# Kernel tuning notes

Measured on AMD Instinct MI355X. Metric: run time of the kernel, lower is better.

The kernel has to match this reference:

```python
import jax, jax.numpy as jnp
import numpy as np

N = 50000      # nodes
E = 800000     # edges
C_IN = 128
C_HID = 128
C_OUT = 128
LN_EPS = 1e-5  # PyG LayerNorm default eps


def setup_inputs() -> dict:
    key = jax.random.key(0)
    ks = jax.random.split(key, 8)
    x = jax.random.normal(ks[0], (N, C_IN), jnp.float32)
    edge_index = jax.random.randint(ks[1], (2, E), 0, N, dtype=jnp.int32)
    s1 = 1.0 / np.sqrt(C_IN)
    s2 = 1.0 / np.sqrt(C_HID)
    return {
        "x": x,
        "edge_index": edge_index,
        "eps1": jnp.float32(1e-4),              # GINConv train_eps init
        "W1": jax.random.normal(ks[2], (C_HID, C_IN), jnp.float32) * s1,
        "b1": jnp.zeros((C_HID,), jnp.float32),
        "ln_w": jnp.ones((C_HID,), jnp.float32),
        "ln_b": jnp.zeros((C_HID,), jnp.float32),
        "prelu_a": jnp.float32(0.25),           # nn.PReLU default single param
        "eps2": jnp.float32(1e-4),
        "W2": jax.random.normal(ks[3], (C_OUT, C_HID), jnp.float32) * s2,
        "b2": jnp.zeros((C_OUT,), jnp.float32),
    }


def _gin_max(x, src, dst, eps, W, b):
    # GINConv(aggr='max'): nn((1+eps)*x + max_{j in N(i)} x_j)
    msg = x[src]                                          # [E, C] gather
    agg = jax.ops.segment_max(msg, dst, num_segments=N)   # [N, C]
    agg = jnp.where(jnp.isfinite(agg), agg, jnp.float32(0.0))  # empty segments -> 0 (PyG fill)
    h = (1.0 + eps) * x + agg
    return h @ W.T + b


def _graph_layernorm(x, w, b):
    # PyG LayerNorm mode='graph', single graph: normalize over ALL nodes & channels
    x = x - jnp.mean(x)
    x = x / (jnp.std(x) + LN_EPS)
    return x * w + b


def reference(x, edge_index, eps1, W1, b1, ln_w, ln_b, prelu_a, eps2, W2, b2):
    src, dst = edge_index[0], edge_index[1]
    h = _gin_max(x, src, dst, eps1, W1, b1)
    h = _graph_layernorm(h, ln_w, ln_b)
    h = jnp.where(h >= 0, h, prelu_a * h)  # PReLU
    return _gin_max(h, src, dst, eps2, W2, b2)
```

## Files before the change

kernel.cpp:

```cpp
#include <hip/hip_runtime.h>
#include <hip/hip_fp16.h>
#include <math.h>

#define NN 50000
#define NE 800000
#define C  128
#define BKT 128
#define NBUK ((NN + BKT - 1) / BKT)
#define ECHUNK 2048
#define NEBLK ((NE + ECHUNK - 1) / ECHUNK)

typedef _Float16 f16x8 __attribute__((ext_vector_type(8)));
typedef float f32x4 __attribute__((ext_vector_type(4)));

__global__ void k_wh(const float* __restrict__ W, _Float16* __restrict__ Wh) {
  int i = blockIdx.x * 256 + threadIdx.x;
  if (i < C * C) Wh[i] = (_Float16)W[i];
}

__global__ __launch_bounds__(256) void k_bh(const int* __restrict__ dst,
                                            int* __restrict__ bh) {
  __shared__ int h[NBUK];
  int t = threadIdx.x;
  for (int i = t; i < NBUK; i += 256) h[i] = 0;
  __syncthreads();
  int base = blockIdx.x * ECHUNK;
  int end = base + ECHUNK; if (end > NE) end = NE;
  for (int e = base + t; e < end; e += 256) atomicAdd(&h[dst[e] >> 7], 1);
  __syncthreads();
  for (int i = t; i < NBUK; i += 256) bh[i * NEBLK + blockIdx.x] = h[i];
}

__global__ __launch_bounds__(256) void k_bscan(int* __restrict__ bh,
                                               int* __restrict__ btot) {
  int b = blockIdx.x, t = threadIdx.x;
  int lane = t & 63, wid = t >> 6;
  __shared__ int wsum[4];
  int carry = 0;
  for (int base = 0; base < NEBLK; base += 256) {
    int i = base + t;
    int v = (i < NEBLK) ? bh[b * NEBLK + i] : 0;
    int incl = v;
    #pragma unroll
    for (int off = 1; off < 64; off <<= 1) {
      int u = __shfl_up(incl, off, 64);
      if (lane >= off) incl += u;
    }
    if (lane == 63) wsum[wid] = incl;
    __syncthreads();
    int woff = 0;
    #pragma unroll
    for (int wI = 0; wI < 4; ++wI) if (wI < wid) woff += wsum[wI];
    if (i < NEBLK) bh[b * NEBLK + i] = carry + woff + incl - v;
    int total = wsum[0] + wsum[1] + wsum[2] + wsum[3];
    __syncthreads();
    carry += total;
  }
  if (t == 0) btot[b] = carry;
}

__global__ __launch_bounds__(256) void k_bbase(const int* __restrict__ btot,
                                               int* __restrict__ bbase,
                                               int* __restrict__ rowstart) {
  int t = threadIdx.x;
  int lane = t & 63, wid = t >> 6;
  __shared__ int wsum[4];
  int carry = 0;
  for (int base = 0; base < NBUK; base += 256) {
    int i = base + t;
    int v = (i < NBUK) ? btot[i] : 0;
    int incl = v;
    #pragma unroll
    for (int off = 1; off < 64; off <<= 1) {
      int u = __shfl_up(incl, off, 64);
      if (lane >= off) incl += u;
    }
    if (lane == 63) wsum[wid] = incl;
    __syncthreads();
    int woff = 0;
    #pragma unroll
    for (int wI = 0; wI < 4; ++wI) if (wI < wid) woff += wsum[wI];
    if (i < NBUK) bbase[i] = carry + woff + incl - v;
    int total = wsum[0] + wsum[1] + wsum[2] + wsum[3];
    __syncthreads();
    carry += total;
  }
  if (t == 0) rowstart[NN] = NE;
}

__global__ __launch_bounds__(256) void k_bscatter(const int* __restrict__ src,
                       const int* __restrict__ dst,
                       const int* __restrict__ bh, const int* __restrict__ bbase,
                       int2* __restrict__ binned) {
  __shared__ int cur[NBUK];
  int t = threadIdx.x, blk = blockIdx.x;
  for (int i = t; i < NBUK; i += 256) cur[i] = bbase[i] + bh[i * NEBLK + blk];
  __syncthreads();
  int base = blk * ECHUNK;
  int end = base + ECHUNK; if (end > NE) end = NE;
  for (int e = base + t; e < end; e += 256) {
    int d = dst[e];
    int pos = atomicAdd(&cur[d >> 7], 1);
    binned[pos] = make_int2(src[e], d);
  }
}

__global__ __launch_bounds__(256) void k_bfill(const int2* __restrict__ binned,
                       const int* __restrict__ bbase, const int* __restrict__ btot,
                       int* __restrict__ rowstart, int* __restrict__ csr) {
  int b = blockIdx.x, t = threadIdx.x;
  __shared__ int hist[BKT];
  __shared__ int cur[BKT];
  __shared__ int wsum[4];
  int s0 = bbase[b];
  int cnt = btot[b];
  if (t < BKT) hist[t] = 0;
  __syncthreads();
  for (int j = t; j < cnt; j += 256) atomicAdd(&hist[binned[s0 + j].y & (BKT - 1)], 1);
  __syncthreads();
  int v = (t < BKT) ? hist[t] : 0;
  int lane = t & 63, wid = t >> 6;
  int incl = v;
  #pragma unroll
  for (int off = 1; off < 64; off <<= 1) {
    int u = __shfl_up(incl, off, 64);
    if (lane >= off) incl += u;
  }
  if (lane == 63) wsum[wid] = incl;
  __syncthreads();
  int woff = 0;
  #pragma unroll
  for (int wI = 0; wI < 4; ++wI) if (wI < wid) woff += wsum[wI];
  int excl = woff + incl - v;
  if (t < BKT) {
    cur[t] = excl;
    int node = b * BKT + t;
    if (node < NN) rowstart[node] = s0 + excl;
  }
  __syncthreads();
  for (int j = t; j < cnt; j += 256) {
    int2 sd = binned[s0 + j];
    int p = atomicAdd(&cur[sd.y & (BKT - 1)], 1);
    csr[s0 + p] = sd.x;
  }
}

__global__ __launch_bounds__(256) void k_tohalf(const float* __restrict__ in,
                                                __half2* __restrict__ o) {
  int i = blockIdx.x * 256 + threadIdx.x;
  if (i < NN * C / 4) {
    float4 v = ((const float4*)in)[i];
    o[2 * i]     = __floats2half2_rn(v.x, v.y);
    o[2 * i + 1] = __floats2half2_rn(v.z, v.w);
  }
}

__global__ __launch_bounds__(256) void k_agg_h(const __half2* __restrict__ xh2,
                       const int* __restrict__ rs, const int* __restrict__ csr,
                       const float* __restrict__ eps_p, __half2* __restrict__ preh2) {
  int wid = threadIdx.x >> 6;
  int lane = threadIdx.x & 63;
  int n = blockIdx.x * 4 + wid;
  if (n >= NN) return;
  int s0 = rs[n], s1 = rs[n + 1];
  float a0 = -INFINITY, a1 = -INFINITY;
  float b0 = -INFINITY, b1 = -INFINITY;
  float c0 = -INFINITY, c1 = -INFINITY;
  float d0 = -INFINITY, d1 = -INFINITY;
  int j = s0;
  for (; j + 3 < s1; j += 4) {
    int e0 = csr[j], e1_ = csr[j + 1], e2 = csr[j + 2], e3 = csr[j + 3];
    __half2 v0 = xh2[(size_t)e0 * 64 + lane];
    __half2 v1 = xh2[(size_t)e1_ * 64 + lane];
    __half2 v2 = xh2[(size_t)e2 * 64 + lane];
    __half2 v3 = xh2[(size_t)e3 * 64 + lane];
    a0 = fmaxf(a0, __low2float(v0)); a1 = fmaxf(a1, __high2float(v0));
    b0 = fmaxf(b0, __low2float(v1)); b1 = fmaxf(b1, __high2float(v1));
    c0 = fmaxf(c0, __low2float(v2)); c1 = fmaxf(c1, __high2float(v2));
    d0 = fmaxf(d0, __low2float(v3)); d1 = fmaxf(d1, __high2float(v3));
  }
  for (; j < s1; ++j) {
    int e0 = csr[j];
    __half2 v0 = xh2[(size_t)e0 * 64 + lane];
    a0 = fmaxf(a0, __low2float(v0)); a1 = fmaxf(a1, __high2float(v0));
  }
  float m0 = fmaxf(fmaxf(a0, b0), fmaxf(c0, d0));
  float m1 = fmaxf(fmaxf(a1, b1), fmaxf(c1, d1));
  if (s1 == s0) { m0 = 0.f; m1 = 0.f; }
  float e1v = 1.0f + eps_p[0];
  __half2 xs = xh2[(size_t)n * 64 + lane];
  float ox = fmaf(e1v, __low2float(xs), m0);
  float oy = fmaf(e1v, __high2float(xs), m1);
  preh2[(size_t)n * 64 + lane] = __floats2half2_rn(ox, oy);
}

__global__ __launch_bounds__(256) void k_gemm_f16(const _Float16* __restrict__ Ah,
                       const _Float16* __restrict__ Wh, const float* __restrict__ bias,
                       float* __restrict__ out) {
  int wid = threadIdx.x >> 6, lane = threadIdx.x & 63;
  int nt = blockIdx.x * 4 + wid;
  if (nt >= NN / 16) return;
  int r = lane & 15;
  int kq = lane >> 4;
  const _Float16* arow = Ah + ((size_t)nt * 16 + r) * C + kq * 8;

  f32x4 acc[8];
  #pragma unroll
  for (int ot = 0; ot < 8; ++ot) {
    float bv = bias[ot * 16 + r];
    f32x4 z = {bv, bv, bv, bv};
    acc[ot] = z;
  }

  #pragma unroll
  for (int kk = 0; kk < 4; ++kk) {
    f16x8 a = *(const f16x8*)(arow + kk * 32);
    #pragma unroll
    for (int ot = 0; ot < 8; ++ot) {
      f16x8 b = *(const f16x8*)(Wh + ((size_t)ot * 16 + r) * C + kk * 32 + kq * 8);
      acc[ot] = __builtin_amdgcn_mfma_f32_16x16x32_f16(a, b, acc[ot], 0, 0, 0);
    }
  }

  size_t nbase = (size_t)nt * 16;
  #pragma unroll
  for (int ot = 0; ot < 8; ++ot) {
    #pragma unroll
    for (int j = 0; j < 4; ++j) {
      out[(nbase + kq * 4 + j) * C + ot * 16 + r] = acc[ot][j];
    }
  }
}

__global__ __launch_bounds__(256) void k_stats(const float* __restrict__ h,
                                               double* __restrict__ st) {
  const int NV = NN * C / 4;
  int stride = gridDim.x * blockDim.x;
  double s = 0.0, ss = 0.0;
  for (int i = blockIdx.x * blockDim.x + threadIdx.x; i < NV; i += stride) {
    float4 v = ((const float4*)h)[i];
    s  += (double)v.x + (double)v.y + (double)v.z + (double)v.w;
    ss += (double)v.x * v.x + (double)v.y * v.y + (double)v.z * v.z + (double)v.w * v.w;
  }
  for (int off = 32; off > 0; off >>= 1) {
    s  += __shfl_down(s, off, 64);
    ss += __shfl_down(ss, off, 64);
  }
  __shared__ double sd[4], ssd[4];
  int wid = threadIdx.x >> 6, lane = threadIdx.x & 63;
  if (lane == 0) { sd[wid] = s; ssd[wid] = ss; }
  __syncthreads();
  if (threadIdx.x == 0) {
    double ts = sd[0] + sd[1] + sd[2] + sd[3];
    double tss = ssd[0] + ssd[1] + ssd[2] + ssd[3];
    atomicAdd(&st[0], ts);
    atomicAdd(&st[1], tss);
  }
}

__global__ void k_final(const double* __restrict__ st, float* __restrict__ scal) {
  double M = (double)NN * C;
  double mean = st[0] / M;
  double var = st[1] / M - mean * mean;
  if (var < 0.0) var = 0.0;
  double stdv = sqrt(var);
  scal[0] = (float)mean;
  scal[1] = (float)(1.0 / (stdv + 1e-5));
}

__global__ __launch_bounds__(256) void k_act(const float* __restrict__ h,
                       const float* __restrict__ scal,
                       const float* __restrict__ lw, const float* __restrict__ lb,
                       const float* __restrict__ a_p, __half2* __restrict__ outh) {
  int i = blockIdx.x * 256 + threadIdx.x;
  if (i >= NN * C / 4) return;
  float mean = scal[0], inv = scal[1], a = a_p[0];
  float4 v = ((const float4*)h)[i];
  int c4 = i & 31;
  float4 w = ((const float4*)lw)[c4];
  float4 b = ((const float4*)lb)[c4];
  float r[4];
  r[0] = (v.x - mean) * inv * w.x + b.x;
  r[1] = (v.y - mean) * inv * w.y + b.y;
  r[2] = (v.z - mean) * inv * w.z + b.z;
  r[3] = (v.w - mean) * inv * w.w + b.w;
  #pragma unroll
  for (int k = 0; k < 4; ++k) r[k] = (r[k] >= 0.f) ? r[k] : a * r[k];
  outh[2 * i]     = __floats2half2_rn(r[0], r[1]);
  outh[2 * i + 1] = __floats2half2_rn(r[2], r[3]);
}

extern "C" void kernel_launch(void* const* d_in, const int* in_sizes, int n_in,
                              void* d_out, int out_size, void* d_ws, size_t ws_size,
                              hipStream_t stream) {
  const float* x    = (const float*)d_in[0];
  const int*   ei   = (const int*)d_in[1];
  const float* eps1 = (const float*)d_in[2];
  const float* W1   = (const float*)d_in[3];
  const float* b1   = (const float*)d_in[4];
  const float* lnw  = (const float*)d_in[5];
  const float* lnb  = (const float*)d_in[6];
  const float* pa   = (const float*)d_in[7];
  const float* eps2 = (const float*)d_in[8];
  const float* W2   = (const float*)d_in[9];
  const float* b2   = (const float*)d_in[10];
  float* out = (float*)d_out;
  const int* srcI = ei;
  const int* dstI = ei + NE;

  char* w = (char*)d_ws;
  float*    B      = (float*)(w);
  __half2*  preh   = (__half2*)(w + 25600000);
  __half2*  xh     = (__half2*)(w + 38400000);
  _Float16* Wh1    = (_Float16*)(w + 51200000);
  _Float16* Wh2    = (_Float16*)(w + 51232768);
  int*      rowst  = (int*)(w + 51265536);
  int*      csr    = (int*)(w + 51465600);
  int2*     binned = (int2*)(w + 54665600);
  int*      bh     = (int*)(w + 61065600);
  int*      btot   = (int*)(w + 61677184);
  int*      bbase  = (int*)(w + 61678848);
  double*   st     = (double*)(w + 61680512);
  float*    scal   = (float*)(w + 61680528);

  hipMemsetAsync(st, 0, 2 * sizeof(double), stream);

  k_wh<<<64, 256, 0, stream>>>(W1, Wh1);
  k_wh<<<64, 256, 0, stream>>>(W2, Wh2);

  k_bh<<<NEBLK, 256, 0, stream>>>(dstI, bh);
  k_bscan<<<NBUK, 256, 0, stream>>>(bh, btot);
  k_bbase<<<1, 256, 0, stream>>>(btot, bbase, rowst);
  k_bscatter<<<NEBLK, 256, 0, stream>>>(srcI, dstI, bh, bbase, binned);
  k_bfill<<<NBUK, 256, 0, stream>>>(binned, bbase, btot, rowst, csr);

  k_tohalf<<<(NN * C / 4 + 255) / 256, 256, 0, stream>>>(x, xh);

  k_agg_h<<<(NN + 3) / 4, 256, 0, stream>>>(xh, rowst, csr, eps1, preh);
  k_gemm_f16<<<(NN / 16 + 3) / 4, 256, 0, stream>>>((const _Float16*)preh, Wh1, b1, B);

  k_stats<<<1024, 256, 0, stream>>>(B, st);
  k_final<<<1, 1, 0, stream>>>(st, scal);
  k_act<<<(NN * C / 4 + 255) / 256, 256, 0, stream>>>(B, scal, lnw, lnb, pa, xh);

  k_agg_h<<<(NN + 3) / 4, 256, 0, stream>>>(xh, rowst, csr, eps2, preh);
  k_gemm_f16<<<(NN / 16 + 3) / 4, 256, 0, stream>>>((const _Float16*)preh, Wh2, b2, out);
}
```

Baseline: 285.1 us.

## Fuse max-aggregation with MFMA GEMM and LayerNorm stats, store hidden in fp16

Merges the gather/max aggregation and the fp16 MFMA GEMM into one kernel. Each block aggregates 16 nodes into a padded LDS tile, then each wave computes two output column tiles. For layer 1 the kernel also accumulates sum and sum-of-squares for the graph LayerNorm and writes the hidden activations in fp16, which removes the separate stats pass and halves the hidden-buffer traffic. The layer-2 output uses nontemporal stores, and the two weight conversions run in one launch. Risks: per-block statistics are now accumulated in float before the double atomics, and the fp16 hidden buffer loses precision before normalisation.

```diff
diff --git a/kernel.cpp b/kernel.cpp
--- a/kernel.cpp
+++ b/kernel.cpp
@@ -9,13 +9,16 @@
 #define NBUK ((NN + BKT - 1) / BKT)
 #define ECHUNK 2048
 #define NEBLK ((NE + ECHUNK - 1) / ECHUNK)
+#define SAP 136
 
 typedef _Float16 f16x8 __attribute__((ext_vector_type(8)));
 typedef float f32x4 __attribute__((ext_vector_type(4)));
 
-__global__ void k_wh(const float* __restrict__ W, _Float16* __restrict__ Wh) {
+__global__ void k_wh(const float* __restrict__ W1, const float* __restrict__ W2,
+                     _Float16* __restrict__ Wh1, _Float16* __restrict__ Wh2) {
   int i = blockIdx.x * 256 + threadIdx.x;
-  if (i < C * C) Wh[i] = (_Float16)W[i];
+  if (i < C * C) Wh1[i] = (_Float16)W1[i];
+  else if (i < 2 * C * C) Wh2[i - C * C] = (_Float16)W2[i - C * C];
 }
 
 __global__ __launch_bounds__(256) void k_bh(const int* __restrict__ dst,
@@ -155,106 +158,101 @@
   }
 }
 
-__global__ __launch_bounds__(256) void k_agg_h(const __half2* __restrict__ xh2,
+template<int MODE>
+__global__ __launch_bounds__(256) void k_agg_gemm(const __half2* __restrict__ xh2,
                        const int* __restrict__ rs, const int* __restrict__ csr,
-                       const float* __restrict__ eps_p, __half2* __restrict__ preh2) {
-  int wid = threadIdx.x >> 6;
-  int lane = threadIdx.x & 63;
-  int n = blockIdx.x * 4 + wid;
-  if (n >= NN) return;
-  int s0 = rs[n], s1 = rs[n + 1];
-  float a0 = -INFINITY, a1 = -INFINITY;
-  float b0 = -INFINITY, b1 = -INFINITY;
-  float c0 = -INFINITY, c1 = -INFINITY;
-  float d0 = -INFINITY, d1 = -INFINITY;
-  int j = s0;
-  for (; j + 3 < s1; j += 4) {
-    int e0 = csr[j], e1_ = csr[j + 1], e2 = csr[j + 2], e3 = csr[j + 3];
-    __half2 v0 = xh2[(size_t)e0 * 64 + lane];
-    __half2 v1 = xh2[(size_t)e1_ * 64 + lane];
-    __half2 v2 = xh2[(size_t)e2 * 64 + lane];
-    __half2 v3 = xh2[(size_t)e3 * 64 + lane];
-    a0 = fmaxf(a0, __low2float(v0)); a1 = fmaxf(a1, __high2float(v0));
-    b0 = fmaxf(b0, __low2float(v1)); b1 = fmaxf(b1, __high2float(v1));
-    c0 = fmaxf(c0, __low2float(v2)); c1 = fmaxf(c1, __high2float(v2));
-    d0 = fmaxf(d0, __low2float(v3)); d1 = fmaxf(d1, __high2float(v3));
-  }
-  for (; j < s1; ++j) {
-    int e0 = csr[j];
-    __half2 v0 = xh2[(size_t)e0 * 64 + lane];
-    a0 = fmaxf(a0, __low2float(v0)); a1 = fmaxf(a1, __high2float(v0));
-  }
-  float m0 = fmaxf(fmaxf(a0, b0), fmaxf(c0, d0));
-  float m1 = fmaxf(fmaxf(a1, b1), fmaxf(c1, d1));
-  if (s1 == s0) { m0 = 0.f; m1 = 0.f; }
+                       const float* __restrict__ eps_p,
+                       const _Float16* __restrict__ Wh, const float* __restrict__ bias,
+                       _Float16* __restrict__ outh, float* __restrict__ outf,
+                       double* __restrict__ st) {
+  __shared__ _Float16 sA[16 * SAP];
+  int t = threadIdx.x, wid = t >> 6, lane = t & 63;
+  int nbase = blockIdx.x * 16;
   float e1v = 1.0f + eps_p[0];
-  __half2 xs = xh2[(size_t)n * 64 + lane];
-  float ox = fmaf(e1v, __low2float(xs), m0);
-  float oy = fmaf(e1v, __high2float(xs), m1);
-  preh2[(size_t)n * 64 + lane] = __floats2half2_rn(ox, oy);
-}
-
-__global__ __launch_bounds__(256) void k_gemm_f16(const _Float16* __restrict__ Ah,
-                       const _Float16* __restrict__ Wh, const float* __restrict__ bias,
-                       float* __restrict__ out) {
-  int wid = threadIdx.x >> 6, lane = threadIdx.x & 63;
-  int nt = blockIdx.x * 4 + wid;
-  if (nt >= NN / 16) return;
-  int r = lane & 15;
-  int kq = lane >> 4;
-  const _Float16* arow = Ah + ((size_t)nt * 16 + r) * C + kq * 8;
-
-  f32x4 acc[8];
-  #pragma unroll
-  for (int ot = 0; ot < 8; ++ot) {
-    float bv = bias[ot * 16 + r];
+
+  #pragma unroll
+  for (int k = 0; k < 4; ++k) {
+    int nl = wid * 4 + k;
+    int n = nbase + nl;
+    int s0 = rs[n], s1 = rs[n + 1];
+    float a0 = -INFINITY, a1 = -INFINITY, b0 = -INFINITY, b1 = -INFINITY;
+    float c0 = -INFINITY, c1 = -INFINITY, d0 = -INFINITY, d1 = -INFINITY;
+    int j = s0;
+    for (; j + 3 < s1; j += 4) {
+      int e0 = csr[j], e1_ = csr[j + 1], e2 = csr[j + 2], e3 = csr[j + 3];
+      __half2 v0 = xh2[(size_t)e0 * 64 + lane];
+      __half2 v1 = xh2[(size_t)e1_ * 64 + lane];
+      __half2 v2 = xh2[(size_t)e2 * 64 + lane];
+      __half2 v3 = xh2[(size_t)e3 * 64 + lane];
+      a0 = fmaxf(a0, __low2float(v0)); a1 = fmaxf(a1, __high2float(v0));
+      b0 = fmaxf(b0, __low2float(v1)); b1 = fmaxf(b1, __high2float(v1));
+      c0 = fmaxf(c0, __low2float(v2)); c1 = fmaxf(c1, __high2float(v2));
+      d0 = fmaxf(d0, __low2float(v3)); d1 = fmaxf(d1, __high2float(v3));
+    }
+    for (; j < s1; ++j) {
+      int e0 = csr[j];
+      __half2 v0 = xh2[(size_t)e0 * 64 + lane];
+      a0 = fmaxf(a0, __low2float(v0)); a1 = fmaxf(a1, __high2float(v0));
+    }
+    float m0 = fmaxf(fmaxf(a0, b0), fmaxf(c0, d0));
+    float m1 = fmaxf(fmaxf(a1, b1), fmaxf(c1, d1));
+    if (s1 == s0) { m0 = 0.f; m1 = 0.f; }
+    __half2 xs = xh2[(size_t)n * 64 + lane];
+    float ox = fmaf(e1v, __low2float(xs), m0);
+    float oy = fmaf(e1v, __high2float(xs), m1);
+    ((__half2*)(sA + nl * SAP))[lane] = __floats2half2_rn(ox, oy);
+  }
+  __syncthreads();
+
+  int r = lane & 15, kq = lane >> 4;
+  const _Float16* arow = sA + r * SAP + kq * 8;
+  f32x4 acc[2];
+  #pragma unroll
+  for (int oi = 0; oi < 2; ++oi) {
+    float bv = bias[(wid * 2 + oi) * 16 + r];
     f32x4 z = {bv, bv, bv, bv};
-    acc[ot] = z;
-  }
-
+    acc[oi] = z;
+  }
   #pragma unroll
   for (int kk = 0; kk < 4; ++kk) {
     f16x8 a = *(const f16x8*)(arow + kk * 32);
     #pragma unroll
-    for (int ot = 0; ot < 8; ++ot) {
+    for (int oi = 0; oi < 2; ++oi) {
+      int ot = wid * 2 + oi;
       f16x8 b = *(const f16x8*)(Wh + ((size_t)ot * 16 + r) * C + kk * 32 + kq * 8);
-      acc[ot] = __builtin_amdgcn_mfma_f32_16x16x32_f16(a, b, acc[ot], 0, 0, 0);
-    }
-  }
-
-  size_t nbase = (size_t)nt * 16;
-  #pragma unroll
-  for (int ot = 0; ot < 8; ++ot) {
+      acc[oi] = __builtin_amdgcn_mfma_f32_16x16x32_f16(a, b, acc[oi], 0, 0, 0);
+    }
+  }
+
+  float s = 0.f, ss = 0.f;
+  #pragma unroll
+  for (int oi = 0; oi < 2; ++oi) {
+    int ot = wid * 2 + oi;
     #pragma unroll
     for (int j = 0; j < 4; ++j) {
-      out[(nbase + kq * 4 + j) * C + ot * 16 + r] = acc[ot][j];
-    }
-  }
-}
-
-__global__ __launch_bounds__(256) void k_stats(const float* __restrict__ h,
-                                               double* __restrict__ st) {
-  const int NV = NN * C / 4;
-  int stride = gridDim.x * blockDim.x;
-  double s = 0.0, ss = 0.0;
-  for (int i = blockIdx.x * blockDim.x + threadIdx.x; i < NV; i += stride) {
-    float4 v = ((const float4*)h)[i];
-    s  += (double)v.x + (double)v.y + (double)v.z + (double)v.w;
-    ss += (double)v.x * v.x + (double)v.y * v.y + (double)v.z * v.z + (double)v.w * v.w;
-  }
-  for (int off = 32; off > 0; off >>= 1) {
-    s  += __shfl_down(s, off, 64);
-    ss += __shfl_down(ss, off, 64);
-  }
-  __shared__ double sd[4], ssd[4];
-  int wid = threadIdx.x >> 6, lane = threadIdx.x & 63;
-  if (lane == 0) { sd[wid] = s; ssd[wid] = ss; }
-  __syncthreads();
-  if (threadIdx.x == 0) {
-    double ts = sd[0] + sd[1] + sd[2] + sd[3];
-    double tss = ssd[0] + ssd[1] + ssd[2] + ssd[3];
-    atomicAdd(&st[0], ts);
-    atomicAdd(&st[1], tss);
+      float v = acc[oi][j];
+      size_t off = (size_t)(nbase + kq * 4 + j) * C + ot * 16 + r;
+      if (MODE == 0) {
+        outh[off] = (_Float16)v;
+        s += v; ss += v * v;
+      } else {
+        __builtin_nontemporal_store(v, &outf[off]);
+      }
+    }
+  }
+  if (MODE == 0) {
+    #pragma unroll
+    for (int off = 32; off > 0; off >>= 1) {
+      s  += __shfl_down(s, off, 64);
+      ss += __shfl_down(ss, off, 64);
+    }
+    __shared__ float sdl[4], ssl[4];
+    if (lane == 0) { sdl[wid] = s; ssl[wid] = ss; }
+    __syncthreads();
+    if (t == 0) {
+      atomicAdd(&st[0], (double)(sdl[0] + sdl[1] + sdl[2] + sdl[3]));
+      atomicAdd(&st[1], (double)(ssl[0] + ssl[1] + ssl[2] + ssl[3]));
+    }
   }
 }
 
@@ -268,26 +266,27 @@
   scal[1] = (float)(1.0 / (stdv + 1e-5));
 }
 
-__global__ __launch_bounds__(256) void k_act(const float* __restrict__ h,
+__global__ __launch_bounds__(256) void k_act_h(const _Float16* __restrict__ h,
                        const float* __restrict__ scal,
                        const float* __restrict__ lw, const float* __restrict__ lb,
-                       const float* __restrict__ a_p, __half2* __restrict__ outh) {
+                       const float* __restrict__ a_p, _Float16* __restrict__ outh) {
   int i = blockIdx.x * 256 + threadIdx.x;
-  if (i >= NN * C / 4) return;
+  if (i >= NN * C / 8) return;
   float mean = scal[0], inv = scal[1], a = a_p[0];
-  float4 v = ((const float4*)h)[i];
-  int c4 = i & 31;
-  float4 w = ((const float4*)lw)[c4];
-  float4 b = ((const float4*)lb)[c4];
-  float r[4];
-  r[0] = (v.x - mean) * inv * w.x + b.x;
-  r[1] = (v.y - mean) * inv * w.y + b.y;
-  r[2] = (v.z - mean) * inv * w.z + b.z;
-  r[3] = (v.w - mean) * inv * w.w + b.w;
-  #pragma unroll
-  for (int k = 0; k < 4; ++k) r[k] = (r[k] >= 0.f) ? r[k] : a * r[k];
-  outh[2 * i]     = __floats2half2_rn(r[0], r[1]);
-  outh[2 * i + 1] = __floats2half2_rn(r[2], r[3]);
+  f16x8 v = ((const f16x8*)h)[i];
+  int c8 = i & 15;
+  float4 w0 = ((const float4*)lw)[c8 * 2], w1 = ((const float4*)lw)[c8 * 2 + 1];
+  float4 b0 = ((const float4*)lb)[c8 * 2], b1 = ((const float4*)lb)[c8 * 2 + 1];
+  float wv[8] = {w0.x, w0.y, w0.z, w0.w, w1.x, w1.y, w1.z, w1.w};
+  float bv[8] = {b0.x, b0.y, b0.z, b0.w, b1.x, b1.y, b1.z, b1.w};
+  f16x8 res;
+  #pragma unroll
+  for (int k = 0; k < 8; ++k) {
+    float r = ((float)v[k] - mean) * inv * wv[k] + bv[k];
+    r = (r >= 0.f) ? r : a * r;
+    res[k] = (_Float16)r;
+  }
+  ((f16x8*)outh)[i] = res;
 }
 
 extern "C" void kernel_launch(void* const* d_in, const int* in_sizes, int n_in,
@@ -309,24 +308,22 @@
   const int* dstI = ei + NE;
 
   char* w = (char*)d_ws;
-  float*    B      = (float*)(w);
-  __half2*  preh   = (__half2*)(w + 25600000);
-  __half2*  xh     = (__half2*)(w + 38400000);
-  _Float16* Wh1    = (_Float16*)(w + 51200000);
-  _Float16* Wh2    = (_Float16*)(w + 51232768);
-  int*      rowst  = (int*)(w + 51265536);
-  int*      csr    = (int*)(w + 51465600);
-  int2*     binned = (int2*)(w + 54665600);
-  int*      bh     = (int*)(w + 61065600);
-  int*      btot   = (int*)(w + 61677184);
-  int*      bbase  = (int*)(w + 61678848);
-  double*   st     = (double*)(w + 61680512);
-  float*    scal   = (float*)(w + 61680528);
+  _Float16* Bh     = (_Float16*)(w);
+  __half2*  xh     = (__half2*)(w + 12800000);
+  _Float16* Wh1    = (_Float16*)(w + 25600000);
+  _Float16* Wh2    = (_Float16*)(w + 25632768);
+  int*      rowst  = (int*)(w + 25665536);
+  int*      csr    = (int*)(w + 25865600);
+  int2*     binned = (int2*)(w + 29065600);
+  int*      bh     = (int*)(w + 35465600);
+  int*      btot   = (int*)(w + 36077184);
+  int*      bbase  = (int*)(w + 36078848);
+  double*   st     = (double*)(w + 36080512);
+  float*    scal   = (float*)(w + 36080528);
 
   hipMemsetAsync(st, 0, 2 * sizeof(double), stream);
 
-  k_wh<<<64, 256, 0, stream>>>(W1, Wh1);
-  k_wh<<<64, 256, 0, stream>>>(W2, Wh2);
+  k_wh<<<128, 256, 0, stream>>>(W1, W2, Wh1, Wh2);
 
   k_bh<<<NEBLK, 256, 0, stream>>>(dstI, bh);
   k_bscan<<<NBUK, 256, 0, stream>>>(bh, btot);
@@ -336,13 +333,13 @@
 
   k_tohalf<<<(NN * C / 4 + 255) / 256, 256, 0, stream>>>(x, xh);
 
-  k_agg_h<<<(NN + 3) / 4, 256, 0, stream>>>(xh, rowst, csr, eps1, preh);
-  k_gemm_f16<<<(NN / 16 + 3) / 4, 256, 0, stream>>>((const _Float16*)preh, Wh1, b1, B);
-
-  k_stats<<<1024, 256, 0, stream>>>(B, st);
+  k_agg_gemm<0><<<NN / 16, 256, 0, stream>>>(xh, rowst, csr, eps1, Wh1, b1,
+                                             Bh, nullptr, st);
+
   k_final<<<1, 1, 0, stream>>>(st, scal);
-  k_act<<<(NN * C / 4 + 255) / 256, 256, 0, stream>>>(B, scal, lnw, lnb, pa, xh);
-
-  k_agg_h<<<(NN + 3) / 4, 256, 0, stream>>>(xh, rowst, csr, eps2, preh);
-  k_gemm_f16<<<(NN / 16 + 3) / 4, 256, 0, stream>>>((const _Float16*)preh, Wh2, b2, out);
-}
+  k_act_h<<<(NN * C / 8 + 255) / 256, 256, 0, stream>>>(Bh, scal, lnw, lnb, pa,
+                                                        (_Float16*)xh);
+
+  k_agg_gemm<1><<<NN / 16, 256, 0, stream>>>(xh, rowst, csr, eps2, Wh2, b2,
+                                             nullptr, out, nullptr);
+}
```

Result: slower. 293.3 us (+2.9%).
